# Optimization experiments

Hardware: AMD Instinct MI355X
Metric: run time of the kernel (lower is better)

## Reference

```python
import jax, jax.numpy as jnp
import numpy as np

N_NODES = 50000
N_EDGES = 600000
N_GRAPHS = 1000


def setup_inputs() -> dict:
    key = jax.random.key(0)
    ks = jax.random.split(key, 16)
    x = jax.random.normal(ks[0], (N_NODES, 37), dtype=jnp.float32)
    edge_index = jax.random.randint(ks[1], (2, N_EDGES), 0, N_NODES, dtype=jnp.int64)
    batch = jnp.sort(jax.random.randint(ks[2], (N_NODES,), 0, N_GRAPHS, dtype=jnp.int64))

    def lin(k, fi, fo):
        s = 1.0 / np.sqrt(fi)
        kw, kb = jax.random.split(k)
        W = jax.random.uniform(kw, (fi, fo), minval=-s, maxval=s, dtype=jnp.float32)
        b = jax.random.uniform(kb, (fo,), minval=-s, maxval=s, dtype=jnp.float32)
        return W, b

    W1, b1 = lin(ks[3], 37, 64)
    W2, b2 = lin(ks[4], 64, 128)
    W3, b3 = lin(ks[5], 128, 64)
    Wf1, bf1 = lin(ks[6], 64, 128)
    Wf2, bf2 = lin(ks[7], 128, 64)
    gamma = jnp.ones((64,), jnp.float32)
    beta = jnp.zeros((64,), jnp.float32)
    return dict(x=x, edge_index=edge_index, batch=batch,
                W1=W1, b1=b1, W2=W2, b2=b2, W3=W3, b3=b3,
                Wf1=Wf1, bf1=bf1, Wf2=Wf2, bf2=bf2, gamma=gamma, beta=beta)


def _gcn_conv(x, W, b, rows, cols, norm, n_nodes):
    # PyG GCNConv: out_i = sum_j norm_ij * (x_j W) + b, over A + I edges
    h = x @ W
    msg = h[rows] * norm[:, None]          # [E+N, F_out] gather
    out = jax.ops.segment_sum(msg, cols, num_segments=n_nodes)  # scatter-add
    return out + b


def reference(x, edge_index, batch,
              W1, b1, W2, b2, W3, b3,
              Wf1, bf1, Wf2, bf2, gamma, beta):
    n = x.shape[0]
    loop = jnp.arange(n, dtype=edge_index.dtype)
    rows = jnp.concatenate([edge_index[0], loop])  # source nodes (+ self loops)
    cols = jnp.concatenate([edge_index[1], loop])  # target nodes
    deg = jax.ops.segment_sum(jnp.ones_like(cols, dtype=x.dtype), cols, num_segments=n)
    dinv = jnp.where(deg > 0, jax.lax.rsqrt(jnp.maximum(deg, 1e-12)), 0.0)
    norm = dinv[rows] * dinv[cols]

    h = jax.nn.relu(_gcn_conv(x, W1, b1, rows, cols, norm, n))
    h = jax.nn.relu(_gcn_conv(h, W2, b2, rows, cols, norm, n))
    h = jax.nn.relu(_gcn_conv(h, W3, b3, rows, cols, norm, n))

    # global mean pool per graph
    sums = jax.ops.segment_sum(h, batch, num_segments=N_GRAPHS)
    cnts = jax.ops.segment_sum(jnp.ones((n,), h.dtype), batch, num_segments=N_GRAPHS)
    g = sums / jnp.maximum(cnts, 1.0)[:, None]

    g = jax.nn.relu(g @ Wf1 + bf1)
    g = jax.nn.relu(g @ Wf2 + bf2)

    mu = jnp.mean(g, axis=-1, keepdims=True)
    var = jnp.mean(jnp.square(g - mu), axis=-1, keepdims=True)
    return (g - mu) * jax.lax.rsqrt(var + 1e-5) * gamma + beta
```

## Files before the change

kernel.cpp:

```cpp
#include <hip/hip_runtime.h>
#include <hip/hip_bf16.h>


#define WAVE 64


__global__ __launch_bounds__(256)
void hist_kernel(const int* __restrict__ cols, int* __restrict__ counts, int E,
                 const int* __restrict__ batch, int* __restrict__ gcnt, int n) {
    int idx = blockIdx.x * 256 + threadIdx.x;
    if (idx < E) {
        atomicAdd(&counts[cols[idx]], 1);
    } else {
        int i = idx - E;
        if (i < n) atomicAdd(&gcnt[batch[i]], 1);
    }
}


__global__ __launch_bounds__(1024)
void scan1_kernel(const int* __restrict__ counts, int* __restrict__ offs,
                  int* __restrict__ bsum, int n) {
    __shared__ int tmp[1024];
    int i = blockIdx.x * 1024 + threadIdx.x;
    int v = (i < n) ? counts[i] : 0;
    tmp[threadIdx.x] = v;
    __syncthreads();
    for (int o = 1; o < 1024; o <<= 1) {
        int x = (threadIdx.x >= o) ? tmp[threadIdx.x - o] : 0;
        __syncthreads();
        tmp[threadIdx.x] += x;
        __syncthreads();
    }
    if (i < n) offs[i] = tmp[threadIdx.x] - v;
    if (threadIdx.x == 1023) bsum[blockIdx.x] = tmp[1023];
}

__global__ __launch_bounds__(1024)
void scan_meta_kernel(int* __restrict__ bsum, int nb,
                      const int* __restrict__ gcnt, int* __restrict__ goff,
                      int ng, int n_nodes) {
    __shared__ int ta[1024];
    __shared__ int tb[1024];
    int t = threadIdx.x;
    int va = (t < nb) ? bsum[t] : 0;
    int vb = (t < ng) ? gcnt[t] : 0;
    ta[t] = va;
    tb[t] = vb;
    __syncthreads();
    for (int o = 1; o < 1024; o <<= 1) {
        int xa = (t >= o) ? ta[t - o] : 0;
        int xb = (t >= o) ? tb[t - o] : 0;
        __syncthreads();
        ta[t] += xa;
        tb[t] += xb;
        __syncthreads();
    }
    if (t < nb) bsum[t] = ta[t] - va;
    if (t < ng) goff[t] = tb[t] - vb;
    if (t == 0) goff[ng] = n_nodes;
}

__global__ __launch_bounds__(256)
void scan3_kernel(int* __restrict__ offs, const int* __restrict__ bsum,
                  const int* __restrict__ counts, float* __restrict__ dinv,
                  int n, int E) {
    int i = blockIdx.x * 256 + threadIdx.x;
    if (i < n) {
        offs[i] += bsum[i >> 10];
        dinv[i] = rsqrtf((float)(counts[i] + 1));
    }
    if (i == 0) offs[n] = E;
}

__global__ __launch_bounds__(256)
void fill_kernel(const int* __restrict__ rows, const int* __restrict__ cols,
                 const int* __restrict__ offs, int* __restrict__ cursor,
                 int* __restrict__ esrc, int E) {
    int e = blockIdx.x * 256 + threadIdx.x;
    if (e >= E) return;
    int r = rows[e], c = cols[e];
    int pos = offs[c] + atomicAdd(&cursor[c], 1);
    esrc[pos] = r;
}


template <int F>
__global__ __launch_bounds__(256)
void scale_kernel(const float* __restrict__ x, const float* __restrict__ dinv,
                  float* __restrict__ g0, int total) {
    int i = blockIdx.x * 256 + threadIdx.x;
    if (i < total) g0[i] = x[i] * dinv[i / F];
}


template <int F>
__global__ __launch_bounds__(256)
void agg_kernel(const float* __restrict__ g, const int* __restrict__ offs,
                const int* __restrict__ esrc, const float* __restrict__ dinv,
                const float* __restrict__ bias, int do_relu,
                float* __restrict__ out, int n) {
    constexpr int J = (F + 63) / 64;
    int wid  = threadIdx.x >> 6;
    int lane = threadIdx.x & 63;
    int node = blockIdx.x * 4 + wid;
    if (node >= n) return;
    float acc0[J], acc1[J], acc2[J], acc3[J];
#pragma unroll
    for (int j = 0; j < J; ++j) {
        int c = lane + 64 * j; if (F % 64 && c >= F) c = F - 1;
        acc0[j] = g[(size_t)node * F + c];
        acc1[j] = 0.f; acc2[j] = 0.f; acc3[j] = 0.f;
    }
    int s = offs[node], e = offs[node + 1];
    int k = s;
    for (; k + 3 < e; k += 4) {
        int s0 = esrc[k], s1 = esrc[k + 1], s2 = esrc[k + 2], s3 = esrc[k + 3];
#pragma unroll
        for (int j = 0; j < J; ++j) {
            int c = lane + 64 * j; if (F % 64 && c >= F) c = F - 1;
            acc0[j] += g[(size_t)s0 * F + c];
            acc1[j] += g[(size_t)s1 * F + c];
            acc2[j] += g[(size_t)s2 * F + c];
            acc3[j] += g[(size_t)s3 * F + c];
        }
    }
    for (; k < e; ++k) {
        int s0 = esrc[k];
#pragma unroll
        for (int j = 0; j < J; ++j) {
            int c = lane + 64 * j; if (F % 64 && c >= F) c = F - 1;
            acc0[j] += g[(size_t)s0 * F + c];
        }
    }
    float dv = dinv[node];
#pragma unroll
    for (int j = 0; j < J; ++j) {
        int c = lane + 64 * j;
        if (F % 64 == 0 || c < F) {
            float v = ((acc0[j] + acc1[j]) + (acc2[j] + acc3[j])) * dv;
            if (bias)    v += bias[c];
            if (do_relu) v = fmaxf(v, 0.f);
            out[(size_t)node * F + c] = v;
        }
    }
}


template <int K, int F>
__global__ __launch_bounds__(256)
void mm_kernel(const float* __restrict__ X, const float* __restrict__ W,
               const float* __restrict__ bias, const float* __restrict__ dscale,
               int do_relu, float* __restrict__ out, int n) {
    constexpr int ROWS = 32;
    constexpr int CG = F / 4;
    __shared__ __align__(16) float Ws[K * F];
    __shared__ __align__(16) float xs[ROWS * K];
    int r0 = blockIdx.x * ROWS;
    for (int i = threadIdx.x; i < K * F; i += 256) Ws[i] = W[i];
    int nrow = n - r0; if (nrow > ROWS) nrow = ROWS;
    const float* Xb = X + (size_t)r0 * K;
    int tot = nrow * K;
    for (int i = threadIdx.x; i < tot; i += 256) xs[i] = Xb[i];
    __syncthreads();
    for (int idx = threadIdx.x; idx < ROWS * CG; idx += 256) {
        int r = idx / CG, cg = idx % CG;
        if (r >= nrow) break;
        float4 acc = {0.f, 0.f, 0.f, 0.f};
#pragma unroll
        for (int k = 0; k < K; ++k) {
            float xv = xs[r * K + k];
            float4 wv = *reinterpret_cast<const float4*>(&Ws[k * F + cg * 4]);
            acc.x += xv * wv.x; acc.y += xv * wv.y;
            acc.z += xv * wv.z; acc.w += xv * wv.w;
        }
        if (bias) {
            const float4 bv = *reinterpret_cast<const float4*>(&bias[cg * 4]);
            acc.x += bv.x; acc.y += bv.y; acc.z += bv.z; acc.w += bv.w;
        }
        if (do_relu) {
            acc.x = fmaxf(acc.x, 0.f); acc.y = fmaxf(acc.y, 0.f);
            acc.z = fmaxf(acc.z, 0.f); acc.w = fmaxf(acc.w, 0.f);
        }
        if (dscale) {
            float dv = dscale[r0 + r];
            acc.x *= dv; acc.y *= dv; acc.z *= dv; acc.w *= dv;
        }
        *reinterpret_cast<float4*>(&out[(size_t)(r0 + r) * F + cg * 4]) = acc;
    }
}


template <int K, int F, int BR, int KC>
__global__ __launch_bounds__(256)
void mm_tiled_kernel(const float* __restrict__ X, const float* __restrict__ W,
                     const float* __restrict__ bias, const float* __restrict__ dscale,
                     int do_relu, float* __restrict__ out, int n) {
    constexpr int TC = F / 4;
    constexpr int TR = 256 / TC;
    constexpr int R  = BR / TR;
    constexpr int XS = KC + 4;
    static_assert(R == 8, "tile math assumes 8 rows/thread");
    static_assert(K % KC == 0 && KC % 4 == 0, "bad K chunking");

    __shared__ __align__(16) float Ws[K * F];
    __shared__ __align__(16) float xs[BR * XS];

    const int t  = threadIdx.x;
    const int tc = t % TC;
    const int tr = t / TC;
    const int r0 = blockIdx.x * BR;

    for (int i = t * 4; i < K * F; i += 1024)
        *reinterpret_cast<float4*>(&Ws[i]) = *reinterpret_cast<const float4*>(&W[i]);

    float4 acc[R];
#pragma unroll
    for (int i = 0; i < R; ++i) acc[i] = float4{0.f, 0.f, 0.f, 0.f};

    for (int kc = 0; kc < K; kc += KC) {
        __syncthreads();
        constexpr int VPR = KC / 4;
        for (int idx = t; idx < BR * VPR; idx += 256) {
            int row = idx / VPR, col = idx % VPR;
            int gr = r0 + row; if (gr >= n) gr = n - 1;
            *reinterpret_cast<float4*>(&xs[row * XS + col * 4]) =
                *reinterpret_cast<const float4*>(&X[(size_t)gr * K + kc + col * 4]);
        }
        __syncthreads();

#pragma unroll 2
        for (int kk = 0; kk < KC; kk += 4) {
            float4 xv[R];
#pragma unroll
            for (int i = 0; i < R; ++i)
                xv[i] = *reinterpret_cast<const float4*>(&xs[(tr + TR * i) * XS + kk]);
            float4 wv[4];
#pragma unroll
            for (int j = 0; j < 4; ++j)
                wv[j] = *reinterpret_cast<const float4*>(&Ws[(kc + kk + j) * F + tc * 4]);
#pragma unroll
            for (int i = 0; i < R; ++i) {
                const float* xp = reinterpret_cast<const float*>(&xv[i]);
#pragma unroll
                for (int j = 0; j < 4; ++j) {
                    float s = xp[j];
                    acc[i].x += s * wv[j].x;
                    acc[i].y += s * wv[j].y;
                    acc[i].z += s * wv[j].z;
                    acc[i].w += s * wv[j].w;
                }
            }
        }
    }

    float4 bv = {0.f, 0.f, 0.f, 0.f};
    if (bias) bv = *reinterpret_cast<const float4*>(&bias[tc * 4]);
#pragma unroll
    for (int i = 0; i < R; ++i) {
        int gr = r0 + tr + TR * i;
        if (gr < n) {
            float4 v = acc[i];
            if (bias) { v.x += bv.x; v.y += bv.y; v.z += bv.z; v.w += bv.w; }
            if (do_relu) {
                v.x = fmaxf(v.x, 0.f); v.y = fmaxf(v.y, 0.f);
                v.z = fmaxf(v.z, 0.f); v.w = fmaxf(v.w, 0.f);
            }
            if (dscale) {
                float dv = dscale[gr];
                v.x *= dv; v.y *= dv; v.z *= dv; v.w *= dv;
            }
            *reinterpret_cast<float4*>(&out[(size_t)gr * F + tc * 4]) = v;
        }
    }
}


__global__ __launch_bounds__(128)
void poolmlp_kernel(const float* __restrict__ h, const int* __restrict__ goff,
                    const float* __restrict__ Wf1, const float* __restrict__ bf1,
                    const float* __restrict__ Wf2, const float* __restrict__ bf2,
                    const float* __restrict__ gamma, const float* __restrict__ beta,
                    float* __restrict__ out) {
    __shared__ float red[128];
    __shared__ float gs[64];
    __shared__ float ts[128];
    int g = blockIdx.x, t = threadIdx.x;
    int f = t & 63, half = t >> 6;
    int s = goff[g], e = goff[g + 1];
    float acc = 0.f;
    for (int i = s + half; i < e; i += 2) acc += h[(size_t)i * 64 + f];
    red[t] = acc;
    __syncthreads();
    if (t < 64) {
        float c = (float)(e - s);
        gs[t] = (red[t] + red[t + 64]) / fmaxf(c, 1.0f);
    }
    __syncthreads();
    float a1 = bf1[t];
    for (int k = 0; k < 64; ++k) a1 += gs[k] * Wf1[k * 128 + t];
    ts[t] = fmaxf(a1, 0.f);
    __syncthreads();
    if (t < 64) {
        float a2 = bf2[t];
        for (int k = 0; k < 128; ++k) a2 += ts[k] * Wf2[k * 64 + t];
        float u = fmaxf(a2, 0.f);
        float mu = u;
        for (int o = 1; o < 64; o <<= 1) mu += __shfl_xor(mu, o);
        mu *= (1.0f / 64.0f);
        float d = u - mu;
        float var = d * d;
        for (int o = 1; o < 64; o <<= 1) var += __shfl_xor(var, o);
        var *= (1.0f / 64.0f);
        out[g * 64 + t] = d * rsqrtf(var + 1e-5f) * gamma[t] + beta[t];
    }
}


extern "C" void kernel_launch(void* const* d_in, const int* in_sizes, int n_in,
                              void* d_out, int out_size, void* d_ws, size_t ws_size,
                              hipStream_t stream) {
    const float* x     = (const float*)d_in[0];
    const int*   eidx  = (const int*)d_in[1];
    const int*   batch = (const int*)d_in[2];
    const float* W1 = (const float*)d_in[3];  const float* b1 = (const float*)d_in[4];
    const float* W2 = (const float*)d_in[5];  const float* b2 = (const float*)d_in[6];
    const float* W3 = (const float*)d_in[7];  const float* b3 = (const float*)d_in[8];
    const float* Wf1 = (const float*)d_in[9];  const float* bf1 = (const float*)d_in[10];
    const float* Wf2 = (const float*)d_in[11]; const float* bf2 = (const float*)d_in[12];
    const float* gamma = (const float*)d_in[13]; const float* beta = (const float*)d_in[14];
    float* out = (float*)d_out;

    const int n  = in_sizes[2];
    const int E  = in_sizes[1] / 2;
    const int ng = out_size / 64;
    const int NB = (n + 1023) / 1024;

    const int* rows = eidx;
    const int* cols = eidx + E;

    size_t off = 0;
    auto carve = [&](size_t bytes) {
        void* p = (char*)d_ws + off;
        off += (bytes + 511) & ~(size_t)511;
        return p;
    };
    int*   counts = (int*)  carve((size_t)n * 4);
    int*   cursor = (int*)  carve((size_t)n * 4);
    int*   gcnt   = (int*)  carve((size_t)(ng + 1) * 4);
    size_t zbytes = off;
    int*   offs   = (int*)  carve((size_t)(n + 1) * 4);
    int*   bsum   = (int*)  carve((size_t)(NB + 1) * 4);
    float* dinv   = (float*)carve((size_t)n * 4);
    int*   esrc   = (int*)  carve((size_t)E * 4);
    int*   goff   = (int*)  carve((size_t)(ng + 1) * 4);
    float* bufA   = (float*)carve((size_t)n * 128 * 4);
    float* bufB   = (float*)carve((size_t)n * 64 * 4);
    (void)ws_size;

    hipMemsetAsync(d_ws, 0, zbytes, stream);

    int gH = (E + n + 255) / 256;
    hist_kernel<<<gH, 256, 0, stream>>>(cols, counts, E, batch, gcnt, n);
    scan1_kernel<<<NB, 1024, 0, stream>>>(counts, offs, bsum, n);
    scan_meta_kernel<<<1, 1024, 0, stream>>>(bsum, NB, gcnt, goff, ng, n);
    scan3_kernel<<<(n + 255) / 256, 256, 0, stream>>>(offs, bsum, counts, dinv, n, E);
    scale_kernel<37><<<(n * 37 + 255) / 256, 256, 0, stream>>>(x, dinv, bufA, n * 37);
    fill_kernel<<<(E + 255) / 256, 256, 0, stream>>>(rows, cols, offs, cursor, esrc, E);

    int gagg = (n + 3) / 4;
    agg_kernel<37><<<gagg, 256, 0, stream>>>(bufA, offs, esrc, dinv, nullptr, 0, bufB, n);
    mm_kernel<37, 64><<<(n + 31) / 32, 256, 0, stream>>>(bufB, W1, b1, dinv, 1, bufA, n);
    agg_kernel<64><<<gagg, 256, 0, stream>>>(bufA, offs, esrc, dinv, nullptr, 0, bufB, n);
    mm_tiled_kernel<64, 128, 64, 64><<<(n + 63) / 64, 256, 0, stream>>>(
        bufB, W2, b2, nullptr, 1, bufA, n);
    mm_tiled_kernel<128, 64, 128, 64><<<(n + 127) / 128, 256, 0, stream>>>(
        bufA, W3, nullptr, dinv, 0, bufB, n);
    agg_kernel<64><<<gagg, 256, 0, stream>>>(bufB, offs, esrc, dinv, b3, 1, bufA, n);

    poolmlp_kernel<<<ng, 128, 0, stream>>>(bufA, goff, Wf1, bf1, Wf2, bf2, gamma, beta, out);
}
```

Measured before the change: 343.0 us.

## Fuse W2/W3 GEMMs in LDS and fold input scaling into aggregation

The two back-to-back dense layers are merged into one kernel that keeps the 128-wide hidden activation in shared memory instead of writing and rereading it from global memory. The separate scale kernel is removed; the first aggregation applies per-source dinv weights on the fly. The aggregation loop is unrolled to eight independent accumulators for more gathers in flight. The trade-off is extra dinv gathers in the first layer, and the fused kernel reads float4 from shared memory at a 130-float row stride, which may break 16-byte alignment.

```diff
diff --git a/kernel.cpp b/kernel.cpp
--- a/kernel.cpp
+++ b/kernel.cpp
@@ -1,8 +1,6 @@
 #include <hip/hip_runtime.h>
 #include <hip/hip_bf16.h>
 
-
-#define WAVE 64
 
 
 __global__ __launch_bounds__(256)
@@ -85,65 +83,48 @@
 }
 
 
-template <int F>
-__global__ __launch_bounds__(256)
-void scale_kernel(const float* __restrict__ x, const float* __restrict__ dinv,
-                  float* __restrict__ g0, int total) {
-    int i = blockIdx.x * 256 + threadIdx.x;
-    if (i < total) g0[i] = x[i] * dinv[i / F];
-}
-
-
-template <int F>
+template <int F, int WSRC>
 __global__ __launch_bounds__(256)
 void agg_kernel(const float* __restrict__ g, const int* __restrict__ offs,
                 const int* __restrict__ esrc, const float* __restrict__ dinv,
                 const float* __restrict__ bias, int do_relu,
                 float* __restrict__ out, int n) {
-    constexpr int J = (F + 63) / 64;
+    static_assert(F <= 64, "one lane per feature");
     int wid  = threadIdx.x >> 6;
     int lane = threadIdx.x & 63;
     int node = blockIdx.x * 4 + wid;
     if (node >= n) return;
-    float acc0[J], acc1[J], acc2[J], acc3[J];
-#pragma unroll
-    for (int j = 0; j < J; ++j) {
-        int c = lane + 64 * j; if (F % 64 && c >= F) c = F - 1;
-        acc0[j] = g[(size_t)node * F + c];
-        acc1[j] = 0.f; acc2[j] = 0.f; acc3[j] = 0.f;
-    }
+    int c = (lane < F) ? lane : (F - 1);
+    float dv = dinv[node];
+    float a0 = (WSRC ? dv : 1.0f) * g[(size_t)node * F + c];
+    float a1 = 0.f, a2 = 0.f, a3 = 0.f, a4 = 0.f, a5 = 0.f, a6 = 0.f, a7 = 0.f;
     int s = offs[node], e = offs[node + 1];
     int k = s;
-    for (; k + 3 < e; k += 4) {
-        int s0 = esrc[k], s1 = esrc[k + 1], s2 = esrc[k + 2], s3 = esrc[k + 3];
-#pragma unroll
-        for (int j = 0; j < J; ++j) {
-            int c = lane + 64 * j; if (F % 64 && c >= F) c = F - 1;
-            acc0[j] += g[(size_t)s0 * F + c];
-            acc1[j] += g[(size_t)s1 * F + c];
-            acc2[j] += g[(size_t)s2 * F + c];
-            acc3[j] += g[(size_t)s3 * F + c];
-        }
+    for (; k + 7 < e; k += 8) {
+        int s0 = esrc[k],     s1 = esrc[k + 1], s2 = esrc[k + 2], s3 = esrc[k + 3];
+        int s4 = esrc[k + 4], s5 = esrc[k + 5], s6 = esrc[k + 6], s7 = esrc[k + 7];
+        float w0 = WSRC ? dinv[s0] : 1.f, w1 = WSRC ? dinv[s1] : 1.f;
+        float w2 = WSRC ? dinv[s2] : 1.f, w3 = WSRC ? dinv[s3] : 1.f;
+        float w4 = WSRC ? dinv[s4] : 1.f, w5 = WSRC ? dinv[s5] : 1.f;
+        float w6 = WSRC ? dinv[s6] : 1.f, w7 = WSRC ? dinv[s7] : 1.f;
+        a0 += w0 * g[(size_t)s0 * F + c];
+        a1 += w1 * g[(size_t)s1 * F + c];
+        a2 += w2 * g[(size_t)s2 * F + c];
+        a3 += w3 * g[(size_t)s3 * F + c];
+        a4 += w4 * g[(size_t)s4 * F + c];
+        a5 += w5 * g[(size_t)s5 * F + c];
+        a6 += w6 * g[(size_t)s6 * F + c];
+        a7 += w7 * g[(size_t)s7 * F + c];
     }
     for (; k < e; ++k) {
         int s0 = esrc[k];
-#pragma unroll
-        for (int j = 0; j < J; ++j) {
-            int c = lane + 64 * j; if (F % 64 && c >= F) c = F - 1;
-            acc0[j] += g[(size_t)s0 * F + c];
-        }
-    }
-    float dv = dinv[node];
-#pragma unroll
-    for (int j = 0; j < J; ++j) {
-        int c = lane + 64 * j;
-        if (F % 64 == 0 || c < F) {
-            float v = ((acc0[j] + acc1[j]) + (acc2[j] + acc3[j])) * dv;
-            if (bias)    v += bias[c];
-            if (do_relu) v = fmaxf(v, 0.f);
-            out[(size_t)node * F + c] = v;
-        }
-    }
+        float w0 = WSRC ? dinv[s0] : 1.f;
+        a0 += w0 * g[(size_t)s0 * F + c];
+    }
+    float v = (((a0 + a1) + (a2 + a3)) + ((a4 + a5) + (a6 + a7))) * dv;
+    if (bias)    v += bias[c];
+    if (do_relu) v = fmaxf(v, 0.f);
+    if (lane < F) out[(size_t)node * F + c] = v;
 }
 
 
@@ -191,87 +172,100 @@
 }
 
 
-template <int K, int F, int BR, int KC>
-__global__ __launch_bounds__(256)
-void mm_tiled_kernel(const float* __restrict__ X, const float* __restrict__ W,
-                     const float* __restrict__ bias, const float* __restrict__ dscale,
-                     int do_relu, float* __restrict__ out, int n) {
-    constexpr int TC = F / 4;
-    constexpr int TR = 256 / TC;
-    constexpr int R  = BR / TR;
-    constexpr int XS = KC + 4;
-    static_assert(R == 8, "tile math assumes 8 rows/thread");
-    static_assert(K % KC == 0 && KC % 4 == 0, "bad K chunking");
-
-    __shared__ __align__(16) float Ws[K * F];
-    __shared__ __align__(16) float xs[BR * XS];
-
+__global__ __launch_bounds__(256)
+void mm23_kernel(const float* __restrict__ X, const float* __restrict__ W2,
+                 const float* __restrict__ b2, const float* __restrict__ W3,
+                 const float* __restrict__ dinv, float* __restrict__ out, int n) {
+    __shared__ __align__(16) float Wbuf[64 * 128];
+    __shared__ __align__(16) float Xbuf[32 * 130];
     const int t  = threadIdx.x;
-    const int tc = t % TC;
-    const int tr = t / TC;
-    const int r0 = blockIdx.x * BR;
-
-    for (int i = t * 4; i < K * F; i += 1024)
-        *reinterpret_cast<float4*>(&Ws[i]) = *reinterpret_cast<const float4*>(&W[i]);
-
-    float4 acc[R];
-#pragma unroll
-    for (int i = 0; i < R; ++i) acc[i] = float4{0.f, 0.f, 0.f, 0.f};
-
-    for (int kc = 0; kc < K; kc += KC) {
-        __syncthreads();
-        constexpr int VPR = KC / 4;
-        for (int idx = t; idx < BR * VPR; idx += 256) {
-            int row = idx / VPR, col = idx % VPR;
-            int gr = r0 + row; if (gr >= n) gr = n - 1;
-            *reinterpret_cast<float4*>(&xs[row * XS + col * 4]) =
-                *reinterpret_cast<const float4*>(&X[(size_t)gr * K + kc + col * 4]);
-        }
-        __syncthreads();
-
+    const int r0 = blockIdx.x * 32;
+
+    for (int i = t * 4; i < 8192; i += 1024)
+        *reinterpret_cast<float4*>(&Wbuf[i]) = *reinterpret_cast<const float4*>(&W2[i]);
+    for (int idx = t; idx < 32 * 16; idx += 256) {
+        int row = idx / 16, col = idx % 16;
+        int gr = r0 + row; if (gr >= n) gr = n - 1;
+        *reinterpret_cast<float4*>(&Xbuf[row * 68 + col * 4]) =
+            *reinterpret_cast<const float4*>(&X[(size_t)gr * 64 + col * 4]);
+    }
+    __syncthreads();
+
+    const int tc = t % 32, tr = t / 32;
+    float4 h2[4];
+#pragma unroll
+    for (int i = 0; i < 4; ++i) h2[i] = float4{0.f, 0.f, 0.f, 0.f};
 #pragma unroll 2
-        for (int kk = 0; kk < KC; kk += 4) {
-            float4 xv[R];
-#pragma unroll
-            for (int i = 0; i < R; ++i)
-                xv[i] = *reinterpret_cast<const float4*>(&xs[(tr + TR * i) * XS + kk]);
-            float4 wv[4];
-#pragma unroll
-            for (int j = 0; j < 4; ++j)
-                wv[j] = *reinterpret_cast<const float4*>(&Ws[(kc + kk + j) * F + tc * 4]);
-#pragma unroll
-            for (int i = 0; i < R; ++i) {
-                const float* xp = reinterpret_cast<const float*>(&xv[i]);
-#pragma unroll
-                for (int j = 0; j < 4; ++j) {
-                    float s = xp[j];
-                    acc[i].x += s * wv[j].x;
-                    acc[i].y += s * wv[j].y;
-                    acc[i].z += s * wv[j].z;
-                    acc[i].w += s * wv[j].w;
-                }
+    for (int kk = 0; kk < 64; kk += 4) {
+        float4 xv[4];
+#pragma unroll
+        for (int i = 0; i < 4; ++i)
+            xv[i] = *reinterpret_cast<const float4*>(&Xbuf[(tr + 8 * i) * 68 + kk]);
+        float4 wv[4];
+#pragma unroll
+        for (int j = 0; j < 4; ++j)
+            wv[j] = *reinterpret_cast<const float4*>(&Wbuf[(kk + j) * 128 + tc * 4]);
+#pragma unroll
+        for (int i = 0; i < 4; ++i) {
+            const float* xp = reinterpret_cast<const float*>(&xv[i]);
+#pragma unroll
+            for (int j = 0; j < 4; ++j) {
+                float s = xp[j];
+                h2[i].x += s * wv[j].x; h2[i].y += s * wv[j].y;
+                h2[i].z += s * wv[j].z; h2[i].w += s * wv[j].w;
             }
         }
     }
-
-    float4 bv = {0.f, 0.f, 0.f, 0.f};
-    if (bias) bv = *reinterpret_cast<const float4*>(&bias[tc * 4]);
-#pragma unroll
-    for (int i = 0; i < R; ++i) {
-        int gr = r0 + tr + TR * i;
-        if (gr < n) {
-            float4 v = acc[i];
-            if (bias) { v.x += bv.x; v.y += bv.y; v.z += bv.z; v.w += bv.w; }
-            if (do_relu) {
-                v.x = fmaxf(v.x, 0.f); v.y = fmaxf(v.y, 0.f);
-                v.z = fmaxf(v.z, 0.f); v.w = fmaxf(v.w, 0.f);
-            }
-            if (dscale) {
-                float dv = dscale[gr];
-                v.x *= dv; v.y *= dv; v.z *= dv; v.w *= dv;
-            }
-            *reinterpret_cast<float4*>(&out[(size_t)gr * F + tc * 4]) = v;
-        }
+    {
+        const float4 bv = *reinterpret_cast<const float4*>(&b2[tc * 4]);
+#pragma unroll
+        for (int i = 0; i < 4; ++i) {
+            h2[i].x = fmaxf(h2[i].x + bv.x, 0.f);
+            h2[i].y = fmaxf(h2[i].y + bv.y, 0.f);
+            h2[i].z = fmaxf(h2[i].z + bv.z, 0.f);
+            h2[i].w = fmaxf(h2[i].w + bv.w, 0.f);
+        }
+    }
+    __syncthreads();
+
+#pragma unroll
+    for (int i = 0; i < 4; ++i)
+        *reinterpret_cast<float4*>(&Xbuf[(tr + 8 * i) * 130 + tc * 4]) = h2[i];
+    for (int i = t * 4; i < 8192; i += 1024)
+        *reinterpret_cast<float4*>(&Wbuf[i]) = *reinterpret_cast<const float4*>(&W3[i]);
+    __syncthreads();
+
+    const int tc3 = t % 16, tr3 = t / 16;
+    float4 q0 = {0.f, 0.f, 0.f, 0.f}, q1 = {0.f, 0.f, 0.f, 0.f};
+#pragma unroll 2
+    for (int k2 = 0; k2 < 128; k2 += 4) {
+        float4 x0 = *reinterpret_cast<const float4*>(&Xbuf[tr3 * 130 + k2]);
+        float4 x1 = *reinterpret_cast<const float4*>(&Xbuf[(tr3 + 16) * 130 + k2]);
+        float4 wv[4];
+#pragma unroll
+        for (int j = 0; j < 4; ++j)
+            wv[j] = *reinterpret_cast<const float4*>(&Wbuf[(k2 + j) * 64 + tc3 * 4]);
+        const float* p0 = reinterpret_cast<const float*>(&x0);
+        const float* p1 = reinterpret_cast<const float*>(&x1);
+#pragma unroll
+        for (int j = 0; j < 4; ++j) {
+            float s0 = p0[j], s1 = p1[j];
+            q0.x += s0 * wv[j].x; q0.y += s0 * wv[j].y;
+            q0.z += s0 * wv[j].z; q0.w += s0 * wv[j].w;
+            q1.x += s1 * wv[j].x; q1.y += s1 * wv[j].y;
+            q1.z += s1 * wv[j].z; q1.w += s1 * wv[j].w;
+        }
+    }
+    int gr0 = r0 + tr3, gr1 = r0 + tr3 + 16;
+    if (gr0 < n) {
+        float dv = dinv[gr0];
+        q0.x *= dv; q0.y *= dv; q0.z *= dv; q0.w *= dv;
+        *reinterpret_cast<float4*>(&out[(size_t)gr0 * 64 + tc3 * 4]) = q0;
+    }
+    if (gr1 < n) {
+        float dv = dinv[gr1];
+        q1.x *= dv; q1.y *= dv; q1.z *= dv; q1.w *= dv;
+        *reinterpret_cast<float4*>(&out[(size_t)gr1 * 64 + tc3 * 4]) = q1;
     }
 }
 
@@ -354,7 +348,7 @@
     float* dinv   = (float*)carve((size_t)n * 4);
     int*   esrc   = (int*)  carve((size_t)E * 4);
     int*   goff   = (int*)  carve((size_t)(ng + 1) * 4);
-    float* bufA   = (float*)carve((size_t)n * 128 * 4);
+    float* bufA   = (float*)carve((size_t)n * 64 * 4);
     float* bufB   = (float*)carve((size_t)n * 64 * 4);
     (void)ws_size;
 
@@ -365,18 +359,14 @@
     scan1_kernel<<<NB, 1024, 0, stream>>>(counts, offs, bsum, n);
     scan_meta_kernel<<<1, 1024, 0, stream>>>(bsum, NB, gcnt, goff, ng, n);
     scan3_kernel<<<(n + 255) / 256, 256, 0, stream>>>(offs, bsum, counts, dinv, n, E);
-    scale_kernel<37><<<(n * 37 + 255) / 256, 256, 0, stream>>>(x, dinv, bufA, n * 37);
     fill_kernel<<<(E + 255) / 256, 256, 0, stream>>>(rows, cols, offs, cursor, esrc, E);
 
     int gagg = (n + 3) / 4;
-    agg_kernel<37><<<gagg, 256, 0, stream>>>(bufA, offs, esrc, dinv, nullptr, 0, bufB, n);
+    agg_kernel<37, 1><<<gagg, 256, 0, stream>>>(x, offs, esrc, dinv, nullptr, 0, bufB, n);
     mm_kernel<37, 64><<<(n + 31) / 32, 256, 0, stream>>>(bufB, W1, b1, dinv, 1, bufA, n);
-    agg_kernel<64><<<gagg, 256, 0, stream>>>(bufA, offs, esrc, dinv, nullptr, 0, bufB, n);
-    mm_tiled_kernel<64, 128, 64, 64><<<(n + 63) / 64, 256, 0, stream>>>(
-        bufB, W2, b2, nullptr, 1, bufA, n);
-    mm_tiled_kernel<128, 64, 128, 64><<<(n + 127) / 128, 256, 0, stream>>>(
-        bufA, W3, nullptr, dinv, 0, bufB, n);
-    agg_kernel<64><<<gagg, 256, 0, stream>>>(bufB, offs, esrc, dinv, b3, 1, bufA, n);
-
-    poolmlp_kernel<<<ng, 128, 0, stream>>>(bufA, goff, Wf1, bf1, Wf2, bf2, gamma, beta, out);
-}
+    agg_kernel<64, 0><<<gagg, 256, 0, stream>>>(bufA, offs, esrc, dinv, nullptr, 0, bufB, n);
+    mm23_kernel<<<(n + 31) / 32, 256, 0, stream>>>(bufB, W2, b2, W3, dinv, bufA, n);
+    agg_kernel<64, 0><<<gagg, 256, 0, stream>>>(bufA, offs, esrc, dinv, b3, 1, bufB, n);
+
+    poolmlp_kernel<<<ng, 128, 0, stream>>>(bufB, goff, Wf1, bf1, Wf2, bf2, gamma, beta, out);
+}
```

After: 332.4 us. 1.03x faster.
